# Kernel tuning notes

Hardware: AMD Instinct MI355X
Metric: run time of the kernel (lower is better)

The kernel has to match this reference:

```python
import jax, jax.numpy as jnp
import numpy as np

EMB = 512
HEADS = 8
B, T = 8, 1024

def setup_inputs() -> dict:
    key = jax.random.key(0)
    ks = jax.random.split(key, 6)
    e, h = EMB, HEADS
    s = 1.0 / np.sqrt(e)
    x = jax.random.normal(ks[0], (B, T, e), dtype=jnp.float32)
    # Linear(emb, emb*heads, bias=False): stored as (e, e*h) for x @ W
    Wk = jax.random.normal(ks[1], (e, e * h), dtype=jnp.float32) * s
    Wq = jax.random.normal(ks[2], (e, e * h), dtype=jnp.float32) * s
    Wv = jax.random.normal(ks[3], (e, e * h), dtype=jnp.float32) * s
    # unifyheads: Linear(heads*emb, emb) with bias
    Wu = jax.random.normal(ks[4], (e * h, e), dtype=jnp.float32) * (1.0 / np.sqrt(e * h))
    bu = jax.random.normal(ks[5], (e,), dtype=jnp.float32) * 0.01
    return {"x": x, "Wk": Wk, "Wq": Wq, "Wv": Wv, "Wu": Wu, "bu": bu}

def reference(x, Wk, Wq, Wv, Wu, bu):
    b, t, e = x.shape
    h = HEADS
    scale = e ** (-0.25)  # applied to both q and k, as in the torch code
    q = (x @ Wq).reshape(b, t, h, e) * scale  # (b,t,h,e)
    k = (x @ Wk).reshape(b, t, h, e) * scale
    v = (x @ Wv).reshape(b, t, h, e)
    dot = jnp.einsum('bqhe,bkhe->bhqk', q, k)      # (b,h,t,t)
    attn = jax.nn.softmax(dot, axis=-1)
    out = jnp.einsum('bhqk,bkhe->bqhe', attn, v)    # (b,t,h,e)
    out = out.reshape(b, t, h * e)
    return out @ Wu + bu                            # (b,t,e)
```

## Files before the change

kernel.cpp:

```cpp
#include <hip/hip_runtime.h>
#include <hip/hip_bf16.h>
#include <cstdint>

typedef __attribute__((ext_vector_type(8))) short bf16x8;
typedef __attribute__((ext_vector_type(4))) float f32x4;

typedef __attribute__((address_space(1))) const void gv_t;
typedef __attribute__((address_space(3))) void lv_t;

__device__ __forceinline__ unsigned short f2b(float f) {
  __hip_bfloat16 h = __float2bfloat16(f);
  return __builtin_bit_cast(unsigned short, h);
}
__device__ __forceinline__ float b2f(unsigned short u) {
  unsigned int x = (unsigned int)u << 16;
  return __builtin_bit_cast(float, x);
}

__global__ __launch_bounds__(256) void k_cast(const float* __restrict__ src,
                                              unsigned short* __restrict__ dst, int n4) {
  int i = blockIdx.x * 256 + threadIdx.x;
  if (i >= n4) return;
  const float4 v = ((const float4*)src)[i];
  ushort4 o;
  o.x = f2b(v.x); o.y = f2b(v.y); o.z = f2b(v.z); o.w = f2b(v.w);
  ((ushort4*)dst)[i] = o;
}

__global__ void k_transpose_cast(const float* __restrict__ src,
                                 unsigned short* __restrict__ dst, int R, int C) {
  __shared__ float tile[32][33];
  const int tx = threadIdx.x, ty = threadIdx.y;
  const int c0 = blockIdx.x * 32, r0 = blockIdx.y * 32;
#pragma unroll
  for (int i = 0; i < 32; i += 8)
    tile[ty + i][tx] = src[(long)(r0 + ty + i) * C + (c0 + tx)];
  __syncthreads();
#pragma unroll
  for (int i = 0; i < 32; i += 8)
    dst[(long)(c0 + ty + i) * R + (r0 + tx)] = f2b(tile[tx][ty + i]);
}

__global__ void k_transpose_cast3(const float* __restrict__ s0, const float* __restrict__ s1,
                                  const float* __restrict__ s2,
                                  unsigned short* __restrict__ dst, int R, int C) {
  const float* src = (blockIdx.z == 0) ? s0 : ((blockIdx.z == 1) ? s1 : s2);
  unsigned short* d = dst + (size_t)blockIdx.z * R * C;
  __shared__ float tile[32][33];
  const int tx = threadIdx.x, ty = threadIdx.y;
  const int c0 = blockIdx.x * 32, r0 = blockIdx.y * 32;
#pragma unroll
  for (int i = 0; i < 32; i += 8)
    tile[ty + i][tx] = src[(long)(r0 + ty + i) * C + (c0 + tx)];
  __syncthreads();
#pragma unroll
  for (int i = 0; i < 32; i += 8)
    d[(long)(c0 + ty + i) * R + (r0 + tx)] = f2b(tile[tx][ty + i]);
}

enum { EPI_QK = 0, EPI_VT = 1 };

#define BAR256() do { asm volatile("" ::: "memory"); __builtin_amdgcn_s_barrier(); asm volatile("" ::: "memory"); } while (0)
#define WAITVM(n) do { asm volatile("s_waitcnt vmcnt(" #n ")" ::: "memory"); __builtin_amdgcn_sched_barrier(0); } while (0)
#define WAITLG() do { asm volatile("s_waitcnt lgkmcnt(0)" ::: "memory"); } while (0)

#define STAGE_A(tt, hw, qq)                                                                     \
  __builtin_amdgcn_global_load_lds(                                                            \
    (gv_t*)(A + (long)(m0 + (hw)*128 + (qq)*64 + rr) * lda + ((tt) << 6) + csw),               \
    (lv_t*)(&L[(((((tt)&1)*2 + (hw))*128 + (qq)*64 + rr))*64 + c0]), 16, 0, 0)

#define STAGE_B(tt, qi)                                                                         \
  __builtin_amdgcn_global_load_lds(                                                            \
    (gv_t*)(Bt + (long)(n0 + (qi)*64 + rr) * ldb + ((tt) << 6) + csw),                         \
    (lv_t*)(&L[32768 + (((((tt)&1)*2 + ((qi)>>1))*128 + ((qi)&1)*64 + rr))*64 + c0]), 16, 0, 0)

#define PHASE(slot, QR, QC) do {                                                                \
    const unsigned short* Abase = &L[((slot)*2 + wr) * 8192];                                   \
    const unsigned short* Bbase = &L[32768 + ((slot)*2 + (wc>>1)) * 8192];                      \
    bf16x8 afr[4][2], bfr[2][2];                                                                \
    _Pragma("unroll")                                                                           \
    for (int fr = 0; fr < 4; ++fr) {                                                            \
      const int rA = (QR)*64 + fr*16 + l15;                                                     \
      _Pragma("unroll")                                                                         \
      for (int kk = 0; kk < 2; ++kk) {                                                          \
        const int cA = (kk*32 + l4*8) ^ ((rA & 7) << 3);                                        \
        afr[fr][kk] = *(const bf16x8*)(Abase + rA*64 + cA);                                     \
      }                                                                                         \
    }                                                                                           \
    _Pragma("unroll")                                                                           \
    for (int fc = 0; fc < 2; ++fc) {                                                            \
      const int rB = (wc&1)*64 + (QC)*32 + fc*16 + l15;                                         \
      _Pragma("unroll")                                                                         \
      for (int kk = 0; kk < 2; ++kk) {                                                          \
        const int cB = (kk*32 + l4*8) ^ ((rB & 7) << 3);                                        \
        bfr[fc][kk] = *(const bf16x8*)(Bbase + rB*64 + cB);                                     \
      }                                                                                         \
    }                                                                                           \
    __builtin_amdgcn_s_setprio(1);                                                              \
    _Pragma("unroll")                                                                           \
    for (int fr = 0; fr < 4; ++fr)                                                              \
      _Pragma("unroll")                                                                         \
      for (int fc = 0; fc < 2; ++fc)                                                            \
        _Pragma("unroll")                                                                       \
        for (int kk = 0; kk < 2; ++kk)                                                          \
          acc[(QR)*4+fr][(QC)*2+fc] = __builtin_amdgcn_mfma_f32_16x16x32_bf16(                  \
              afr[fr][kk], bfr[fc][kk], acc[(QR)*4+fr][(QC)*2+fc], 0, 0, 0);                    \
    __builtin_amdgcn_s_setprio(0);                                                              \
  } while (0)

template <int EPI>
__global__ __launch_bounds__(512)
void k_gemm256(const unsigned short* __restrict__ A, const unsigned short* __restrict__ Bt,
               void* __restrict__ Cv, int K, int lda, int ldb, float scale) {
  const int m0 = blockIdx.y * 256;
  const int n0 = blockIdx.x * 256;
  __shared__ __align__(16) unsigned short L[65536];
  const int tid = threadIdx.x;
  const int lane = tid & 63;
  const int wid = tid >> 6;
  const int wr = wid >> 2;
  const int wc = wid & 3;
  const int l15 = lane & 15;
  const int l4 = lane >> 4;
  const int rr = tid >> 3;
  const int c0 = (tid & 7) * 8;
  const int csw = c0 ^ ((rr & 7) << 3);

  f32x4 acc[8][4] = {};
  const int NT = K >> 6;

  STAGE_A(0, 0, 0); STAGE_A(0, 1, 0); STAGE_A(0, 0, 1); STAGE_A(0, 1, 1);
  STAGE_B(0, 0); STAGE_B(0, 1); STAGE_B(0, 2); STAGE_B(0, 3);
  if (NT > 1) {
    STAGE_A(1, 0, 0); STAGE_A(1, 1, 0);
    WAITVM(2);
  } else {
    WAITVM(0);
  }
  __builtin_amdgcn_s_barrier();
  asm volatile("" ::: "memory");

  for (int t = 0; t < NT; ++t) {
    const int slot = t & 1;
    if (t + 1 < NT) { STAGE_A(t + 1, 0, 1); STAGE_A(t + 1, 1, 1); }
    PHASE(slot, 0, 0);
    BAR256();
    if (t + 1 < NT) { STAGE_B(t + 1, 0); STAGE_B(t + 1, 1); }
    PHASE(slot, 0, 1);
    BAR256();
    if (t + 1 < NT) { STAGE_B(t + 1, 2); STAGE_B(t + 1, 3); }
    if (t + 2 < NT) { STAGE_A(t + 2, 0, 0); STAGE_A(t + 2, 1, 0); }
    PHASE(slot, 1, 0);
    BAR256();
    PHASE(slot, 1, 1);
    if (t + 1 < NT) {
      if (t + 2 < NT) WAITVM(2);
      else            WAITVM(0);
      __builtin_amdgcn_s_barrier();
      asm volatile("" ::: "memory");
    }
  }

#pragma unroll
  for (int i = 0; i < 8; ++i) {
#pragma unroll
    for (int j = 0; j < 4; ++j) {
#pragma unroll
      for (int r = 0; r < 4; ++r) {
        const int row = m0 + wr * 128 + i * 16 + l4 * 4 + r;
        const int col = n0 + wc * 64 + j * 16 + l15;
        const float v = acc[i][j][r];
        if (EPI == EPI_QK) {
          unsigned short* o = (unsigned short*)Cv;
          const int sec = col >> 12;
          const int cc = col & 4095;
          const long addr = (long)sec * 33554432 +
              ((long)((row >> 10) * 8 + (cc >> 9)) * 1024 + (row & 1023)) * 512 + (cc & 511);
          o[addr] = f2b(v * scale);
        } else {
          unsigned short* o = (unsigned short*)Cv;
          const long addr = (long)((col >> 10) * 8 + (row >> 9)) * 524288 +
                            (long)(row & 511) * 1024 + (col & 1023);
          o[addr] = f2b(v);
        }
      }
    }
  }
}

#define VSWZ(e) ((((e) & 3) ^ (((e) >> 2) & 3)))

__device__ __forceinline__ void stage_k(const unsigned short* kg, unsigned short* dst,
                                        int c, int w, int lane) {
#pragma unroll
  for (int i = 0; i < 4; ++i) {
    const int row = i * 8 + w;
    __builtin_amdgcn_global_load_lds(
        (gv_t*)(kg + (size_t)(c * 32 + row) * 512 + 8 * (lane ^ (row & 7))),
        (lv_t*)(dst + row * 512 + lane * 8), 16, 0, 0);
  }
}
__device__ __forceinline__ void stage_v(const unsigned short* vg, unsigned short* dst,
                                        int c, int w, int lane) {
#pragma unroll
  for (int i = 0; i < 4; ++i) {
    const int r0 = i * 128 + w * 16;
    const int e = r0 + (lane >> 2);
    __builtin_amdgcn_global_load_lds(
        (gv_t*)(vg + (size_t)e * 1024 + c * 32 + 8 * ((lane & 3) ^ VSWZ(e))),
        (lv_t*)(dst + r0 * 32 + lane * 8), 16, 0, 0);
  }
}

__global__ __launch_bounds__(512)
void k_attn(unsigned short* __restrict__ q,
            const unsigned short* __restrict__ k,
            const unsigned short* __restrict__ vt)
{
  __shared__ __align__(16) unsigned short Ks[2][16384];
  __shared__ __align__(16) unsigned short Vs[2][16384];
  __shared__ __align__(16) unsigned short Es[2][2560];
  const int bid = blockIdx.x;
  const int head = (bid & 7) * 8 + ((bid >> 3) >> 4);
  const int qt = (bid >> 3) & 15;
  const int tid = threadIdx.x;
  const int w = tid >> 6, lane = tid & 63;
  const int l15 = lane & 15, l4 = lane >> 4;
  const int qf = w & 3, kf = w >> 2;

  unsigned short* qg = q + (size_t)(head * 1024 + qt * 64) * 512;
  const unsigned short* kg = k + (size_t)head * 524288;
  const unsigned short* vg = vt + (size_t)head * 524288;

  const int qrow = qf * 16 + l15;
  const int krow = kf * 16 + l15;

  bf16x8 q_r[16];
#pragma unroll
  for (int ks = 0; ks < 16; ++ks)
    q_r[ks] = *(const bf16x8*)(qg + (size_t)qrow * 512 + (size_t)(ks * 4 + l4) * 8);

  stage_k(kg, &Ks[0][0], 0, w, lane);
  stage_v(vg, &Vs[0][0], 0, w, lane);
  stage_k(kg, &Ks[1][0], 1, w, lane);

  f32x4 acc[4][4] = {};
  float partial = 0.f;
  const int erow = tid >> 3;
  const int ej = tid & 7;
  const int eidx = 40 * erow + ej * 4;

  for (int c = 0; c < 32; ++c) {
    unsigned short* KsC = &Ks[c & 1][0];
    unsigned short* VsC = &Vs[c & 1][0];
    unsigned short* EsC = &Es[c & 1][0];
    if (c < 31) { WAITVM(4); } else { WAITVM(0); }
    WAITLG();
    __builtin_amdgcn_s_barrier();
    asm volatile("" ::: "memory");
    if (c + 1 < 32) stage_v(vg, &Vs[(c + 1) & 1][0], c + 1, w, lane);
    f32x4 sacc0 = {0.f, 0.f, 0.f, 0.f};
    f32x4 sacc1 = {0.f, 0.f, 0.f, 0.f};
    __builtin_amdgcn_s_setprio(1);
#pragma unroll
    for (int ks = 0; ks < 16; ks += 2) {
      bf16x8 bk0 = *(const bf16x8*)(&KsC[krow * 512 + 8 * ((ks * 4 + l4) ^ (krow & 7))]);
      sacc0 = __builtin_amdgcn_mfma_f32_16x16x32_bf16(q_r[ks], bk0, sacc0, 0, 0, 0);
      bf16x8 bk1 = *(const bf16x8*)(&KsC[krow * 512 + 8 * (((ks + 1) * 4 + l4) ^ (krow & 7))]);
      sacc1 = __builtin_amdgcn_mfma_f32_16x16x32_bf16(q_r[ks + 1], bk1, sacc1, 0, 0, 0);
    }
    __builtin_amdgcn_s_setprio(0);
#pragma unroll
    for (int r = 0; r < 4; ++r) {
      const int qq = qf * 16 + l4 * 4 + r;
      const int kk2 = kf * 16 + l15;
      EsC[40 * qq + kk2] = f2b(__expf(sacc0[r] + sacc1[r]));
    }
    WAITLG();
    __builtin_amdgcn_s_barrier();
    asm volatile("" ::: "memory");
    if (c + 2 < 32) stage_k(kg, KsC, c + 2, w, lane);
    {
      const ushort4 ev = *(const ushort4*)(&EsC[eidx]);
      partial += (b2f(ev.x) + b2f(ev.y)) + (b2f(ev.z) + b2f(ev.w));
    }
    bf16x8 bv[4];
#pragma unroll
    for (int cf = 0; cf < 4; ++cf) {
      const int e = w * 64 + cf * 16 + l15;
      bv[cf] = *(const bf16x8*)(&VsC[e * 32 + 8 * (l4 ^ VSWZ(e))]);
    }
    __builtin_amdgcn_s_setprio(1);
#pragma unroll
    for (int qf2 = 0; qf2 < 4; ++qf2) {
      const int qq = qf2 * 16 + l15;
      bf16x8 ae = *(const bf16x8*)(&EsC[40 * qq + 8 * l4]);
#pragma unroll
      for (int cf = 0; cf < 4; ++cf)
        acc[qf2][cf] = __builtin_amdgcn_mfma_f32_16x16x32_bf16(ae, bv[cf], acc[qf2][cf], 0, 0, 0);
    }
    __builtin_amdgcn_s_setprio(0);
  }

  __syncthreads();
  float* fs = (float*)&Ks[0][0];
  fs[tid] = partial;
  __syncthreads();
  if (tid < 64) {
    float s = 0.f;
#pragma unroll
    for (int j = 0; j < 8; ++j) s += fs[tid * 8 + j];
    fs[512 + tid] = 1.0f / s;
  }
  __syncthreads();

#pragma unroll
  for (int qf2 = 0; qf2 < 4; ++qf2) {
#pragma unroll
    for (int r = 0; r < 4; ++r) {
      const int qq = qf2 * 16 + l4 * 4 + r;
      const float iv = fs[512 + qq];
#pragma unroll
      for (int cf = 0; cf < 4; ++cf) {
        const int e = w * 64 + cf * 16 + l15;
        qg[(size_t)qq * 512 + e] = f2b(acc[qf2][cf][r] * iv);
      }
    }
  }
}

__global__ __launch_bounds__(256)
void k_gemm_out(const unsigned short* __restrict__ A, const unsigned short* __restrict__ Bt,
                float* __restrict__ C, const float* __restrict__ bias) {
  const int m0 = blockIdx.y * 128;
  const int n0 = blockIdx.x * 128;
  __shared__ __align__(16) unsigned short As[2][128 * 32];
  __shared__ __align__(16) unsigned short Bs[2][128 * 32];
  const int tid = threadIdx.x;
  const int lane = tid & 63;
  const int wm = ((tid >> 6) >> 1) * 64;
  const int wn = ((tid >> 6) & 1) * 64;
  const int srow = tid >> 2;
  const int scol = (tid & 3) * 8;
  f32x4 acc[4][4] = {};

  const int row1 = m0 + srow, row2 = row1 + 64;
  const size_t hb1 = (size_t)(row1 >> 10) * 8 * 524288 + (size_t)(row1 & 1023) * 512;
  const size_t hb2 = (size_t)(row2 >> 10) * 8 * 524288 + (size_t)(row2 & 1023) * 512;
  const unsigned short* gb = Bt + (size_t)(n0 + srow) * 4096 + scol;

#define STAGEO(buf, k0) do {                                                                          \
    const size_t koffA = (size_t)((k0) >> 9) * 524288 + ((k0) & 511) + scol;                          \
    __builtin_amdgcn_global_load_lds((gv_t*)(A + hb1 + koffA), (lv_t*)(&As[buf][tid * 8]), 16, 0, 0);  \
    __builtin_amdgcn_global_load_lds((gv_t*)(A + hb2 + koffA), (lv_t*)(&As[buf][tid * 8 + 2048]), 16, 0, 0); \
    __builtin_amdgcn_global_load_lds((gv_t*)(gb + (k0)), (lv_t*)(&Bs[buf][tid * 8]), 16, 0, 0);        \
    __builtin_amdgcn_global_load_lds((gv_t*)(gb + 64L * 4096 + (k0)), (lv_t*)(&Bs[buf][tid * 8 + 2048]), 16, 0, 0); \
  } while (0)

  STAGEO(0, 0);
  for (int k0 = 0; k0 < 4096; k0 += 32) {
    const int cur = (k0 >> 5) & 1;
    __syncthreads();
    if (k0 + 32 < 4096) { STAGEO(cur ^ 1, k0 + 32); }
    const unsigned short* ap = &As[cur][(wm + (lane & 15)) * 32 + (lane >> 4) * 8];
    const unsigned short* bp = &Bs[cur][(wn + (lane & 15)) * 32 + (lane >> 4) * 8];
    bf16x8 fa[4], fb[4];
#pragma unroll
    for (int i = 0; i < 4; ++i) fa[i] = *(const bf16x8*)(ap + i * 16 * 32);
#pragma unroll
    for (int i = 0; i < 4; ++i) fb[i] = *(const bf16x8*)(bp + i * 16 * 32);
#pragma unroll
    for (int mi = 0; mi < 4; ++mi)
#pragma unroll
      for (int ni = 0; ni < 4; ++ni)
        acc[mi][ni] = __builtin_amdgcn_mfma_f32_16x16x32_bf16(fa[mi], fb[ni], acc[mi][ni], 0, 0, 0);
  }
#undef STAGEO

#pragma unroll
  for (int mi = 0; mi < 4; ++mi) {
#pragma unroll
    for (int ni = 0; ni < 4; ++ni) {
#pragma unroll
      for (int r = 0; r < 4; ++r) {
        const int row = m0 + wm + mi * 16 + ((lane >> 4) * 4 + r);
        const int col = n0 + wn + ni * 16 + (lane & 15);
        C[(long)row * 512 + col] = acc[mi][ni][r] + bias[col];
      }
    }
  }
}

extern "C" void kernel_launch(void* const* d_in, const int* in_sizes, int n_in,
                              void* d_out, int out_size, void* d_ws, size_t ws_size,
                              hipStream_t stream) {
  const float* x  = (const float*)d_in[0];
  const float* Wk = (const float*)d_in[1];
  const float* Wq = (const float*)d_in[2];
  const float* Wv = (const float*)d_in[3];
  const float* Wu = (const float*)d_in[4];
  const float* bu = (const float*)d_in[5];
  float* out = (float*)d_out;
  char* ws = (char*)d_ws;

  const size_t NEED = 226492416;
  if (ws_size < NEED) return;

  unsigned short* wut   = (unsigned short*)(ws + 0);
  unsigned short* wtqkv = (unsigned short*)(ws + 4194304);
  unsigned short* xb    = (unsigned short*)(ws + 16777216);
  unsigned short* qb    = (unsigned short*)(ws + 25165824);
  unsigned short* kb    = qb + 33554432;
  unsigned short* vtb   = qb + 67108864;

  const float s4 = 0.21022410381342865f;

  k_cast<<<4096, 256, 0, stream>>>(x, xb, 1048576);
  k_transpose_cast3<<<dim3(128, 16, 3), dim3(32, 8), 0, stream>>>(Wq, Wk, Wv, wtqkv, 512, 4096);
  k_transpose_cast<<<dim3(16, 128), dim3(32, 8), 0, stream>>>(Wu, wut, 4096, 512);

  k_gemm256<EPI_QK><<<dim3(32, 32, 1), 512, 0, stream>>>(xb, wtqkv, qb, 512, 512, 512, s4);
  k_gemm256<EPI_VT><<<dim3(32, 16, 1), 512, 0, stream>>>(wtqkv + 4194304, xb, vtb, 512, 512, 512, 1.0f);

  k_attn<<<1024, 512, 0, stream>>>(qb, kb, vtb);

  k_gemm_out<<<dim3(4, 64, 1), 256, 0, stream>>>(qb, wut, out, bu);
}
```

Measured before the change: 470.4 us.

## Halve attention query tile and load V directly from global into registers

The attention kernel now handles 32 query rows per block with 256 threads instead of 64 rows with 512 threads, doubling the grid. V fragments are read straight from global memory into registers each chunk, so the double-buffered V staging in LDS is gone and LDS use drops by roughly half. A barrier is added at the end of each chunk iteration. This aims at higher occupancy and less LDS traffic, but it doubles total K/V reads across blocks and turns V into per-lane strided global loads. K synchronization now depends on implicit vmcnt waits, which may not be enough to cover other waves' staged rows.

Measured after the change: 546.0 us. +16.1%, slower.

```diff
diff --git a/kernel.cpp b/kernel.cpp
--- a/kernel.cpp
+++ b/kernel.cpp
@@ -188,47 +188,33 @@
   }
 }
 
-#define VSWZ(e) ((((e) & 3) ^ (((e) >> 2) & 3)))
-
-__device__ __forceinline__ void stage_k(const unsigned short* kg, unsigned short* dst,
-                                        int c, int w, int lane) {
-#pragma unroll
-  for (int i = 0; i < 4; ++i) {
-    const int row = i * 8 + w;
+__device__ __forceinline__ void stage_k4(const unsigned short* kg, unsigned short* dst,
+                                         int c, int w, int lane) {
+#pragma unroll
+  for (int i = 0; i < 8; ++i) {
+    const int row = i * 4 + w;
     __builtin_amdgcn_global_load_lds(
         (gv_t*)(kg + (size_t)(c * 32 + row) * 512 + 8 * (lane ^ (row & 7))),
         (lv_t*)(dst + row * 512 + lane * 8), 16, 0, 0);
   }
 }
-__device__ __forceinline__ void stage_v(const unsigned short* vg, unsigned short* dst,
-                                        int c, int w, int lane) {
-#pragma unroll
-  for (int i = 0; i < 4; ++i) {
-    const int r0 = i * 128 + w * 16;
-    const int e = r0 + (lane >> 2);
-    __builtin_amdgcn_global_load_lds(
-        (gv_t*)(vg + (size_t)e * 1024 + c * 32 + 8 * ((lane & 3) ^ VSWZ(e))),
-        (lv_t*)(dst + r0 * 32 + lane * 8), 16, 0, 0);
-  }
-}
-
-__global__ __launch_bounds__(512)
+
+__global__ __launch_bounds__(256)
 void k_attn(unsigned short* __restrict__ q,
             const unsigned short* __restrict__ k,
             const unsigned short* __restrict__ vt)
 {
   __shared__ __align__(16) unsigned short Ks[2][16384];
-  __shared__ __align__(16) unsigned short Vs[2][16384];
-  __shared__ __align__(16) unsigned short Es[2][2560];
+  __shared__ __align__(16) unsigned short Es[2][1280];
   const int bid = blockIdx.x;
-  const int head = (bid & 7) * 8 + ((bid >> 3) >> 4);
-  const int qt = (bid >> 3) & 15;
+  const int head = (bid & 7) * 8 + ((bid >> 3) >> 5);
+  const int qt = (bid >> 3) & 31;
   const int tid = threadIdx.x;
   const int w = tid >> 6, lane = tid & 63;
   const int l15 = lane & 15, l4 = lane >> 4;
-  const int qf = w & 3, kf = w >> 2;
-
-  unsigned short* qg = q + (size_t)(head * 1024 + qt * 64) * 512;
+  const int qf = w & 1, kf = w >> 1;
+
+  unsigned short* qg = q + (size_t)(head * 1024 + qt * 32) * 512;
   const unsigned short* kg = k + (size_t)head * 524288;
   const unsigned short* vg = vt + (size_t)head * 524288;
 
@@ -240,11 +226,13 @@
   for (int ks = 0; ks < 16; ++ks)
     q_r[ks] = *(const bf16x8*)(qg + (size_t)qrow * 512 + (size_t)(ks * 4 + l4) * 8);
 
-  stage_k(kg, &Ks[0][0], 0, w, lane);
-  stage_v(vg, &Vs[0][0], 0, w, lane);
-  stage_k(kg, &Ks[1][0], 1, w, lane);
-
-  f32x4 acc[4][4] = {};
+  stage_k4(kg, &Ks[0][0], 0, w, lane);
+  stage_k4(kg, &Ks[1][0], 1, w, lane);
+  WAITVM(8);
+  __builtin_amdgcn_s_barrier();
+  asm volatile("" ::: "memory");
+
+  f32x4 acc[2][8] = {};
   float partial = 0.f;
   const int erow = tid >> 3;
   const int ej = tid & 7;
@@ -252,13 +240,13 @@
 
   for (int c = 0; c < 32; ++c) {
     unsigned short* KsC = &Ks[c & 1][0];
-    unsigned short* VsC = &Vs[c & 1][0];
     unsigned short* EsC = &Es[c & 1][0];
-    if (c < 31) { WAITVM(4); } else { WAITVM(0); }
-    WAITLG();
-    __builtin_amdgcn_s_barrier();
-    asm volatile("" ::: "memory");
-    if (c + 1 < 32) stage_v(vg, &Vs[(c + 1) & 1][0], c + 1, w, lane);
+    bf16x8 bv[8];
+#pragma unroll
+    for (int cf = 0; cf < 8; ++cf) {
+      const int e = w * 128 + cf * 16 + l15;
+      bv[cf] = *(const bf16x8*)(vg + (size_t)e * 1024 + c * 32 + l4 * 8);
+    }
     f32x4 sacc0 = {0.f, 0.f, 0.f, 0.f};
     f32x4 sacc1 = {0.f, 0.f, 0.f, 0.f};
     __builtin_amdgcn_s_setprio(1);
@@ -279,50 +267,47 @@
     WAITLG();
     __builtin_amdgcn_s_barrier();
     asm volatile("" ::: "memory");
-    if (c + 2 < 32) stage_k(kg, KsC, c + 2, w, lane);
+    if (c + 2 < 32) stage_k4(kg, KsC, c + 2, w, lane);
     {
       const ushort4 ev = *(const ushort4*)(&EsC[eidx]);
       partial += (b2f(ev.x) + b2f(ev.y)) + (b2f(ev.z) + b2f(ev.w));
     }
-    bf16x8 bv[4];
-#pragma unroll
-    for (int cf = 0; cf < 4; ++cf) {
-      const int e = w * 64 + cf * 16 + l15;
-      bv[cf] = *(const bf16x8*)(&VsC[e * 32 + 8 * (l4 ^ VSWZ(e))]);
-    }
     __builtin_amdgcn_s_setprio(1);
 #pragma unroll
-    for (int qf2 = 0; qf2 < 4; ++qf2) {
+    for (int qf2 = 0; qf2 < 2; ++qf2) {
       const int qq = qf2 * 16 + l15;
       bf16x8 ae = *(const bf16x8*)(&EsC[40 * qq + 8 * l4]);
 #pragma unroll
-      for (int cf = 0; cf < 4; ++cf)
+      for (int cf = 0; cf < 8; ++cf)
         acc[qf2][cf] = __builtin_amdgcn_mfma_f32_16x16x32_bf16(ae, bv[cf], acc[qf2][cf], 0, 0, 0);
     }
     __builtin_amdgcn_s_setprio(0);
+    asm volatile("" ::: "memory");
+    __builtin_amdgcn_s_barrier();
+    asm volatile("" ::: "memory");
   }
 
   __syncthreads();
   float* fs = (float*)&Ks[0][0];
   fs[tid] = partial;
   __syncthreads();
-  if (tid < 64) {
+  if (tid < 32) {
     float s = 0.f;
 #pragma unroll
     for (int j = 0; j < 8; ++j) s += fs[tid * 8 + j];
-    fs[512 + tid] = 1.0f / s;
+    fs[256 + tid] = 1.0f / s;
   }
   __syncthreads();
 
 #pragma unroll
-  for (int qf2 = 0; qf2 < 4; ++qf2) {
+  for (int qf2 = 0; qf2 < 2; ++qf2) {
 #pragma unroll
     for (int r = 0; r < 4; ++r) {
       const int qq = qf2 * 16 + l4 * 4 + r;
-      const float iv = fs[512 + qq];
-#pragma unroll
-      for (int cf = 0; cf < 4; ++cf) {
-        const int e = w * 64 + cf * 16 + l15;
+      const float iv = fs[256 + qq];
+#pragma unroll
+      for (int cf = 0; cf < 8; ++cf) {
+        const int e = w * 128 + cf * 16 + l15;
         qg[(size_t)qq * 512 + e] = f2b(acc[qf2][cf][r] * iv);
       }
     }
@@ -422,7 +407,7 @@
   k_gemm256<EPI_QK><<<dim3(32, 32, 1), 512, 0, stream>>>(xb, wtqkv, qb, 512, 512, 512, s4);
   k_gemm256<EPI_VT><<<dim3(32, 16, 1), 512, 0, stream>>>(wtqkv + 4194304, xb, vtb, 512, 512, 512, 1.0f);
 
-  k_attn<<<1024, 512, 0, stream>>>(qb, kb, vtb);
+  k_attn<<<2048, 256, 0, stream>>>(qb, kb, vtb);
 
   k_gemm_out<<<dim3(4, 64, 1), 256, 0, stream>>>(qb, wut, out, bu);
 }
```
